# Kernel optimization log

Measured on AMD Instinct MI355X. Metric: run time of the kernel, lower is better.

## Reference

```python
import jax, jax.numpy as jnp
import numpy as np

DIM = 512; H = 8; DH = 64; M = 256; ITERS = 6; K = 33  # residual conv kernel


def _pinv(x, iters=ITERS):
    # Moore-Penrose iterative pseudo-inverse (lucidrains moore_penrose_iter_pinv)
    abs_x = jnp.abs(x)
    denom = abs_x.sum(-1).max() * abs_x.sum(-2).max()  # global max of col/row sums
    z = jnp.swapaxes(x, -1, -2) / denom
    I = jnp.eye(x.shape[-1], dtype=x.dtype)
    for _ in range(iters):
        xz = x @ z
        z = 0.25 * z @ (13. * I - xz @ (15. * I - xz @ (7. * I - xz)))
    return z


def setup_inputs() -> dict:
    key = jax.random.key(0)
    ks = jax.random.split(key, 5)
    b, n = 4, 4096
    inner = H * DH
    x = jax.random.normal(ks[0], (b, n, DIM), jnp.float32)
    ln_g = jnp.ones((DIM,), jnp.float32)
    ln_b = jnp.zeros((DIM,), jnp.float32)
    w_qkv = jax.random.normal(ks[1], (DIM, 3 * inner), jnp.float32) / np.sqrt(DIM).astype(np.float32)
    w_out = jax.random.normal(ks[2], (inner, DIM), jnp.float32) / np.sqrt(inner).astype(np.float32)
    b_out = jnp.zeros((DIM,), jnp.float32)
    res_w = jax.random.normal(ks[3], (H, K), jnp.float32) * 0.02  # depthwise conv weight per head
    return {"x": x, "ln_g": ln_g, "ln_b": ln_b, "w_qkv": w_qkv,
            "w_out": w_out, "b_out": b_out, "res_w": res_w}


def reference(x, ln_g, ln_b, w_qkv, w_out, b_out, res_w):
    b, n, d = x.shape
    # LayerNorm (eps=1e-5, biased variance, like torch)
    mu = x.mean(-1, keepdims=True)
    var = ((x - mu) ** 2).mean(-1, keepdims=True)
    xn = (x - mu) * jax.lax.rsqrt(var + 1e-5) * ln_g + ln_b
    # QKV projection, no bias
    qkv = xn @ w_qkv  # [b, n, 3*h*dh]
    q, k, v = jnp.split(qkv, 3, axis=-1)
    tohd = lambda t: t.reshape(b, n, H, DH).transpose(0, 2, 1, 3)  # b h n d
    q = tohd(q) * (DH ** -0.5)
    k = tohd(k)
    v = tohd(v)
    # landmarks: mean over consecutive blocks of l = n // M (n divisible by M here)
    l = n // M
    q_l = q.reshape(b, H, M, l, DH).mean(3)  # b h m d
    k_l = k.reshape(b, H, M, l, DH).mean(3)
    attn1 = jax.nn.softmax(jnp.einsum('bhid,bhjd->bhij', q, k_l), axis=-1)   # b h n m
    attn2 = jax.nn.softmax(jnp.einsum('bhid,bhjd->bhij', q_l, k_l), axis=-1)  # b h m m
    attn3 = jax.nn.softmax(jnp.einsum('bhid,bhjd->bhij', q_l, k), axis=-1)   # b h m n
    out = (attn1 @ _pinv(attn2)) @ (attn3 @ v)  # b h n dh
    # depthwise residual conv over sequence dim (Conv2d(heads, heads, (33,1), groups=heads))
    res = jax.lax.conv_general_dilated(
        v, res_w.reshape(H, 1, K, 1), (1, 1), ((K // 2, K // 2), (0, 0)),
        feature_group_count=H, dimension_numbers=('NCHW', 'OIHW', 'NCHW'))
    out = out + res
    # merge heads + output projection (dropout is identity at eval)
    out = out.transpose(0, 2, 1, 3).reshape(b, n, H * DH) @ w_out + b_out
    # TransLayer residual
    return x + out
```

## Files before the change

### kernel.cpp

```cpp
#include <hip/hip_runtime.h>
#include <hip/hip_bf16.h>

#define SEQ    4096
#define NBAT   4
#define NHEAD  8
#define NBH    32
#define DMODEL 512
#define DHEAD  64
#define NLM    256
#define NSP    4

typedef __attribute__((ext_vector_type(8))) short s8v;
typedef __attribute__((ext_vector_type(4))) float f4v;

__device__ __forceinline__ float b2f(unsigned short u){
  union { unsigned int i; float f; } v; v.i = ((unsigned int)u) << 16; return v.f;
}
__device__ __forceinline__ unsigned short f2b(float f){
  union { float f; unsigned int i; } v; v.f = f;
  unsigned int r = v.i + 0x7fffu + ((v.i >> 16) & 1u);
  return (unsigned short)(r >> 16);
}
__device__ __forceinline__ s8v ldg8(const unsigned short* p){
  return *reinterpret_cast<const s8v*>(p);
}
__device__ __forceinline__ f4v mfma16(s8v a, s8v b, f4v c){
  return __builtin_amdgcn_mfma_f32_16x16x32_bf16(a, b, c, 0, 0, 0);
}
__device__ __forceinline__ f4v zero4(){ f4v z; z[0]=0.f; z[1]=0.f; z[2]=0.f; z[3]=0.f; return z; }
__device__ __forceinline__ void gload16(const unsigned short* g, unsigned short* l){
  __builtin_amdgcn_global_load_lds((const __attribute__((address_space(1))) unsigned int*)g,
                                   (__attribute__((address_space(3))) unsigned int*)l, 16, 0, 0);
}

__global__ void k_prep(const float* __restrict__ wqkv, const float* __restrict__ wout,
                       unsigned short* __restrict__ wqkvT, unsigned short* __restrict__ woutT,
                       unsigned int* __restrict__ denomU){
  int t = blockIdx.x*256 + threadIdx.x;
  if (t == 0) denomU[0] = 0u;
  if (t < 786432){ int kk = t/1536, n = t%1536; wqkvT[(size_t)n*512 + kk] = f2b(wqkv[t]); }
  else { int t2 = t - 786432; if (t2 < 262144){ int kk = t2/512, n = t2%512; woutT[(size_t)n*512 + kk] = f2b(wout[t2]); } }
}

__global__ __launch_bounds__(256) void k_ln(const float* __restrict__ x, const float* __restrict__ g,
                                            const float* __restrict__ be, unsigned short* __restrict__ xn){
  int row = blockIdx.x*4 + (threadIdx.x>>6);
  int l = threadIdx.x & 63;
  const float* xr = x + (size_t)row*DMODEL;
  float4 a = *(const float4*)(xr + l*4);
  float4 b = *(const float4*)(xr + 256 + l*4);
  float s = a.x+a.y+a.z+a.w + b.x+b.y+b.z+b.w;
  float q = a.x*a.x+a.y*a.y+a.z*a.z+a.w*a.w + b.x*b.x+b.y*b.y+b.z*b.z+b.w*b.w;
  #pragma unroll
  for (int m=1;m<64;m<<=1){ s += __shfl_xor(s,m); q += __shfl_xor(q,m); }
  float mean = s*(1.f/DMODEL);
  float rstd = rsqrtf(q*(1.f/DMODEL) - mean*mean + 1e-5f);
  int c0 = l*4, c1 = 256 + l*4;
  float av[4] = {a.x,a.y,a.z,a.w}, bv[4] = {b.x,b.y,b.z,b.w};
  ushort4 u0, u1;
  unsigned short* p0 = (unsigned short*)&u0; unsigned short* p1 = (unsigned short*)&u1;
  #pragma unroll
  for (int e=0;e<4;++e){
    p0[e] = f2b((av[e]-mean)*rstd*g[c0+e] + be[c0+e]);
    p1[e] = f2b((bv[e]-mean)*rstd*g[c1+e] + be[c1+e]);
  }
  *(ushort4*)(xn + (size_t)row*DMODEL + c0) = u0;
  *(ushort4*)(xn + (size_t)row*DMODEL + c1) = u1;
}

__device__ __forceinline__ void gemm512v2(const unsigned short* __restrict__ A, const unsigned short* __restrict__ B,
                                          int m0, int n0, int t, unsigned short* lA, unsigned short* lB,
                                          f4v acc[4][4]){
  int w = t>>6, l = t&63;
  int wm = (w&1)*64, wn = (w>>1)*64;
  int g = l>>4, qi = l&15;
  int rs = (w<<4) + (l>>2);
  int s0 = l&3;
  int c0 = ((s0 ^ ((rs>>1)&3)) << 3);
  int r1 = rs + 64;
  int c1 = ((s0 ^ ((r1>>1)&3)) << 3);
  const unsigned short* gA0 = A + (size_t)(m0+rs)*DMODEL + c0;
  const unsigned short* gA1 = A + (size_t)(m0+r1)*DMODEL + c1;
  const unsigned short* gB0 = B + (size_t)(n0+rs)*DMODEL + c0;
  const unsigned short* gB1 = B + (size_t)(n0+r1)*DMODEL + c1;
  unsigned short* dA0 = lA + (w<<9);
  unsigned short* dA1 = lA + 2048 + (w<<9);
  unsigned short* dB0 = lB + (w<<9);
  unsigned short* dB1 = lB + 2048 + (w<<9);
  int aofs[4], bofs[4];
  #pragma unroll
  for (int i=0;i<4;++i){
    int ra = wm + i*16 + qi;
    aofs[i] = ra*32 + ((g ^ ((ra>>1)&3))<<3);
    int rb = wn + i*16 + qi;
    bofs[i] = rb*32 + ((g ^ ((rb>>1)&3))<<3);
  }
  for (int ks=0; ks<16; ++ks){
    gload16(gA0, dA0); gload16(gA1, dA1);
    gload16(gB0, dB0); gload16(gB1, dB1);
    gA0 += 32; gA1 += 32; gB0 += 32; gB1 += 32;
    __syncthreads();
    s8v af[4], bf[4];
    #pragma unroll
    for (int i=0;i<4;++i) af[i] = *(s8v*)&lA[aofs[i]];
    #pragma unroll
    for (int j=0;j<4;++j) bf[j] = *(s8v*)&lB[bofs[j]];
    #pragma unroll
    for (int i=0;i<4;++i)
      #pragma unroll
      for (int j=0;j<4;++j) acc[i][j] = mfma16(af[i], bf[j], acc[i][j]);
    __syncthreads();
  }
}

__global__ __launch_bounds__(256) void k_gqkv(const unsigned short* __restrict__ xn, const unsigned short* __restrict__ wT,
                                              unsigned short* __restrict__ q, unsigned short* __restrict__ k,
                                              unsigned short* __restrict__ v, unsigned short* __restrict__ vT){
  __shared__ __align__(16) unsigned short lA[4096], lB[4096];
  int b0 = blockIdx.x;
  int bid = (b0 & 7) * 192 + (b0 >> 3);
  int mblk = bid/12, nblk = bid%12;
  int m0 = mblk*128, n0 = nblk*128;
  int t = threadIdx.x;
  f4v acc[4][4];
  #pragma unroll
  for (int i=0;i<4;++i)
    #pragma unroll
    for (int j=0;j<4;++j) acc[i][j] = zero4();
  gemm512v2(xn, wT, m0, n0, t, lA, lB, acc);
  int w = t>>6, l = t&63; int wm = (w&1)*64, wn = (w>>1)*64;
  int part = nblk >> 2;
  int coff = (nblk & 3) * 128;
  unsigned short* dst = (part==0) ? q : (part==1) ? k : v;
  float scale = (part==0) ? 0.125f : 1.f;
  #pragma unroll
  for (int i=0;i<4;++i)
  #pragma unroll
  for (int j=0;j<4;++j){
    int colg = coff + wn + j*16 + (l&15);
    int h = colg>>6, c = colg&63;
    #pragma unroll
    for (int r=0;r<4;++r){
      int rowg = m0 + wm + i*16 + ((l>>4)<<2) + r;
      int b = rowg>>12, n = rowg&4095;
      unsigned short val = f2b(acc[i][j][r]*scale);
      dst[ (((size_t)(b*NHEAD + h))*SEQ + n)*DHEAD + c ] = val;
      if (part == 2)
        vT[ (((size_t)(b*NHEAD + h))*DHEAD + c)*SEQ + n ] = val;
    }
  }
}

__global__ __launch_bounds__(256) void k_gout(const unsigned short* __restrict__ ao, const unsigned short* __restrict__ wT,
                                              const float* __restrict__ x, const float* __restrict__ bo,
                                              float* __restrict__ out){
  __shared__ __align__(16) unsigned short lA[4096], lB[4096];
  int b0 = blockIdx.x;
  int bid = (b0 & 7) * 64 + (b0 >> 3);
  int mblk = bid>>2, nblk = bid&3;
  int m0 = mblk*128, n0 = nblk*128;
  int t = threadIdx.x;
  f4v acc[4][4];
  #pragma unroll
  for (int i=0;i<4;++i)
    #pragma unroll
    for (int j=0;j<4;++j) acc[i][j] = zero4();
  gemm512v2(ao, wT, m0, n0, t, lA, lB, acc);
  int w = t>>6, l = t&63; int wm = (w&1)*64, wn = (w>>1)*64;
  #pragma unroll
  for (int i=0;i<4;++i)
  #pragma unroll
  for (int j=0;j<4;++j){
    int colg = n0 + wn + j*16 + (l&15);
    #pragma unroll
    for (int r=0;r<4;++r){
      int rowg = m0 + wm + i*16 + ((l>>4)<<2) + r;
      size_t ad = (size_t)rowg*DMODEL + colg;
      out[ad] = acc[i][j][r] + x[ad] + bo[colg];
    }
  }
}

__global__ void k_lmk(const unsigned short* __restrict__ q, const unsigned short* __restrict__ k,
                      unsigned short* __restrict__ ql, unsigned short* __restrict__ kl){
  int tg = blockIdx.x*256 + threadIdx.x;
  int c4 = (tg&15)*4, m = (tg>>4)&255, bh = tg>>12;
  const unsigned short* qb = q + ((size_t)bh*SEQ + m*16)*DHEAD + c4;
  const unsigned short* kb = k + ((size_t)bh*SEQ + m*16)*DHEAD + c4;
  float s0=0.f,s1=0.f,s2=0.f,s3=0.f, t0=0.f,t1=0.f,t2=0.f,t3=0.f;
  #pragma unroll
  for (int j=0;j<16;++j){
    ushort4 uq = *(const ushort4*)(qb + (size_t)j*DHEAD);
    ushort4 uk = *(const ushort4*)(kb + (size_t)j*DHEAD);
    s0+=b2f(uq.x); s1+=b2f(uq.y); s2+=b2f(uq.z); s3+=b2f(uq.w);
    t0+=b2f(uk.x); t1+=b2f(uk.y); t2+=b2f(uk.z); t3+=b2f(uk.w);
  }
  ushort4 oq, ok;
  oq.x=f2b(s0*(1.f/16.f)); oq.y=f2b(s1*(1.f/16.f)); oq.z=f2b(s2*(1.f/16.f)); oq.w=f2b(s3*(1.f/16.f));
  ok.x=f2b(t0*(1.f/16.f)); ok.y=f2b(t1*(1.f/16.f)); ok.z=f2b(t2*(1.f/16.f)); ok.w=f2b(t3*(1.f/16.f));
  *(ushort4*)(ql + ((size_t)bh*NLM + m)*DHEAD + c4) = oq;
  *(ushort4*)(kl + ((size_t)bh*NLM + m)*DHEAD + c4) = ok;
}

__global__ __launch_bounds__(512) void k_attn2(const unsigned short* __restrict__ ql, const unsigned short* __restrict__ kl,
                                               unsigned short* __restrict__ a2, unsigned short* __restrict__ a2t,
                                               unsigned int* __restrict__ denomU){
  __shared__ float cs[256];
  int bh = blockIdx.x; int t = threadIdx.x; int w = t>>6, l = t&63;
  const unsigned short* Q = ql + (size_t)bh*NLM*DHEAD;
  const unsigned short* K = kl + (size_t)bh*NLM*DHEAD;
  f4v acc[2][16];
  #pragma unroll
  for (int i=0;i<2;++i)
    #pragma unroll
    for (int j=0;j<16;++j) acc[i][j] = zero4();
  int m0 = w*32;
  #pragma unroll
  for (int ks=0; ks<2; ++ks){
    int kk = ks*32 + ((l>>4)<<3);
    s8v af0 = ldg8(&Q[(size_t)(m0 + (l&15))*DHEAD + kk]);
    s8v af1 = ldg8(&Q[(size_t)(m0 + 16 + (l&15))*DHEAD + kk]);
    #pragma unroll
    for (int j=0;j<16;++j){
      s8v bf = ldg8(&K[(size_t)(j*16 + (l&15))*DHEAD + kk]);
      acc[0][j] = mfma16(af0, bf, acc[0][j]);
      acc[1][j] = mfma16(af1, bf, acc[1][j]);
    }
  }
  #pragma unroll
  for (int i=0;i<2;++i)
  #pragma unroll
  for (int r=0;r<4;++r){
    float mx = -1e30f;
    #pragma unroll
    for (int j=0;j<16;++j) mx = fmaxf(mx, acc[i][j][r]);
    #pragma unroll
    for (int mm=1;mm<16;mm<<=1) mx = fmaxf(mx, __shfl_xor(mx,mm));
    float sm = 0.f;
    #pragma unroll
    for (int j=0;j<16;++j){ float p = __expf(acc[i][j][r]-mx); acc[i][j][r]=p; sm += p; }
    #pragma unroll
    for (int mm=1;mm<16;mm<<=1) sm += __shfl_xor(sm,mm);
    float inv = 1.f/sm;
    #pragma unroll
    for (int j=0;j<16;++j) acc[i][j][r] *= inv;
  }
  for (int e=t; e<256; e+=512) cs[e] = 0.f;
  __syncthreads();
  size_t b0 = (size_t)bh*NLM*NLM;
  #pragma unroll
  for (int i=0;i<2;++i)
  #pragma unroll
  for (int j=0;j<16;++j){
    int col = j*16 + (l&15);
    int rowb = m0 + i*16 + ((l>>4)<<2);
    float csp = 0.f;
    #pragma unroll
    for (int r=0;r<4;++r){
      float p = acc[i][j][r];
      unsigned short pb = f2b(p);
      a2 [b0 + (size_t)(rowb+r)*NLM + col] = pb;
      a2t[b0 + (size_t)col*NLM + rowb + r] = pb;
      csp += p;
    }
    csp += __shfl_xor(csp, 16); csp += __shfl_xor(csp, 32);
    if ((l>>4) == 0) atomicAdd(&cs[col], csp);
  }
  __syncthreads();
  if (t < 256) atomicMax(denomU, __float_as_uint(cs[t]));
}

__global__ __launch_bounds__(256) void k_a3w2p(const unsigned short* __restrict__ ql, const unsigned short* __restrict__ kb,
                                               const unsigned short* __restrict__ vT,
                                               float* __restrict__ po, float* __restrict__ pm, float* __restrict__ pd){
  __shared__ __align__(16) unsigned short Ks[256*64];
  __shared__ __align__(16) unsigned short Vs[64*256];
  int bid = blockIdx.x;
  int ksp = bid & 3;
  int qp  = (bid >> 2) & 3;
  int bh  = bid >> 4;
  int t = threadIdx.x, w = t>>6, l = t&63;
  int q0 = qp*64 + w*16;
  int g = l>>4, qi = l&15;
  const unsigned short* Q = ql + ((size_t)bh*NLM + q0)*DHEAD;
  const unsigned short* K = kb + (size_t)bh*SEQ*DHEAD;
  const unsigned short* V = vT + (size_t)bh*DHEAD*SEQ;
  s8v bq0 = ldg8(&Q[(size_t)qi*DHEAD + g*8]);
  s8v bq1 = ldg8(&Q[(size_t)qi*DHEAD + 32 + g*8]);
  float m_run = -1e30f, den = 0.f;
  f4v oacc[4];
  #pragma unroll
  for (int j=0;j<4;++j) oacc[j] = zero4();
  int sl0 = ((g&1)*2)*16 + qi;
  int jsel = g>>1;
  for (int kc = ksp*4; kc < ksp*4+4; ++kc){
    const unsigned short* Kc = K + (size_t)kc*256*DHEAD;
    #pragma unroll
    for (int it2=0; it2<8; ++it2){
      int cid = it2*256 + t;
      int row = cid>>3, cl = cid&7;
      gload16(&Kc[(size_t)(row<<6) + ((cl^(row&7))<<3)], Ks + it2*2048 + w*512);
      int row2 = cid>>5, cl2 = cid&31;
      gload16(&V[(size_t)row2*SEQ + kc*256 + ((cl2^(row2&7))<<3)], Vs + it2*2048 + 16384 - 16384 + w*512 + 0);
    }
    __syncthreads();
    f4v acc[16];
    #pragma unroll
    for (int j=0;j<16;++j) acc[j] = zero4();
    #pragma unroll
    for (int ks=0;ks<2;++ks){
      s8v bq = (ks==0) ? bq0 : bq1;
      #pragma unroll
      for (int j=0;j<16;++j){
        int r = j*16+qi;
        s8v ak = *(s8v*)&Ks[(size_t)(r<<6) + (((ks*4+g) ^ (qi&7))<<3)];
        acc[j] = mfma16(ak, bq, acc[j]);
      }
    }
    float cm = -1e30f;
    #pragma unroll
    for (int j=0;j<16;++j)
      cm = fmaxf(cm, fmaxf(fmaxf(acc[j][0],acc[j][1]), fmaxf(acc[j][2],acc[j][3])));
    cm = fmaxf(cm, __shfl_xor(cm,16));
    cm = fmaxf(cm, __shfl_xor(cm,32));
    float nm = fmaxf(m_run, cm);
    float f = __expf(m_run - nm);
    m_run = nm;
    float ls = 0.f;
    unsigned int pku[32];
    #pragma unroll
    for (int j=0;j<16;++j){
      float p0 = __expf(acc[j][0]-nm), p1 = __expf(acc[j][1]-nm);
      float p2 = __expf(acc[j][2]-nm), p3 = __expf(acc[j][3]-nm);
      ls += (p0+p1)+(p2+p3);
      pku[2*j+0] = (unsigned int)f2b(p0) | ((unsigned int)f2b(p1)<<16);
      pku[2*j+1] = (unsigned int)f2b(p2) | ((unsigned int)f2b(p3)<<16);
    }
    den = den*f + ls;
    float fr0 = __shfl(f, g*4+0, 64), fr1 = __shfl(f, g*4+1, 64);
    float fr2 = __shfl(f, g*4+2, 64), fr3 = __shfl(f, g*4+3, 64);
    #pragma unroll
    for (int j=0;j<4;++j){
      oacc[j][0]*=fr0; oacc[j][1]*=fr1; oacc[j][2]*=fr2; oacc[j][3]*=fr3;
    }
    #pragma unroll
    for (int ks=0;ks<8;++ks){
      unsigned int w0a = (unsigned int)__shfl((int)pku[4*ks+0], sl0, 64);
      unsigned int w1a = (unsigned int)__shfl((int)pku[4*ks+1], sl0, 64);
      unsigned int w0b = (unsigned int)__shfl((int)pku[4*ks+2], sl0, 64);
      unsigned int w1b = (unsigned int)__shfl((int)pku[4*ks+3], sl0, 64);
      unsigned int w2a = (unsigned int)__shfl((int)pku[4*ks+0], sl0+16, 64);
      unsigned int w3a = (unsigned int)__shfl((int)pku[4*ks+1], sl0+16, 64);
      unsigned int w2b = (unsigned int)__shfl((int)pku[4*ks+2], sl0+16, 64);
      unsigned int w3b = (unsigned int)__shfl((int)pku[4*ks+3], sl0+16, 64);
      unsigned int wv0 = jsel ? w0b : w0a;
      unsigned int wv1 = jsel ? w1b : w1a;
      unsigned int wv2 = jsel ? w2b : w2a;
      unsigned int wv3 = jsel ? w3b : w3a;
      s8v af;
      af[0] = (short)(wv0&0xffff); af[1] = (short)(wv0>>16);
      af[2] = (short)(wv1&0xffff); af[3] = (short)(wv1>>16);
      af[4] = (short)(wv2&0xffff); af[5] = (short)(wv2>>16);
      af[6] = (short)(wv3&0xffff); af[7] = (short)(wv3>>16);
      int ch = ks*4 + g;
      #pragma unroll
      for (int j=0;j<4;++j){
        int r = j*16+qi;
        s8v bu = *(s8v*)&Vs[(size_t)(r<<8) + ((ch ^ (qi&7))<<3)];
        oacc[j] = mfma16(af, bu, oacc[j]);
      }
    }
    __syncthreads();
  }
  den += __shfl_xor(den,16); den += __shfl_xor(den,32);
  #pragma unroll
  for (int j=0;j<4;++j)
    #pragma unroll
    for (int r=0;r<4;++r)
      po[(((size_t)(ksp*NBH + bh))*NLM + q0 + g*4 + r)*DHEAD + j*16 + qi] = oacc[j][r];
  if (g == 0){
    pm[(size_t)(ksp*NBH + bh)*NLM + q0 + qi] = m_run;
    pd[(size_t)(ksp*NBH + bh)*NLM + q0 + qi] = den;
  }
}

__global__ __launch_bounds__(256) void k_a3c(const float* __restrict__ po, const float* __restrict__ pm,
                                             const float* __restrict__ pd, unsigned short* __restrict__ w2t){
  int tg = blockIdx.x*256 + threadIdx.x;
  int bh = tg >> 12; int c = (tg >> 6) & 63; int r4 = (tg & 63) << 2;
  ushort4 ov;
  unsigned short* op = (unsigned short*)&ov;
  #pragma unroll
  for (int rr=0; rr<4; ++rr){
    int row = r4 + rr;
    float m[NSP];
    float gm = -1e30f;
    #pragma unroll
    for (int s=0;s<NSP;++s){ m[s] = pm[(size_t)(s*NBH+bh)*NLM + row]; gm = fmaxf(gm, m[s]); }
    float den = 0.f, o = 0.f;
    #pragma unroll
    for (int s=0;s<NSP;++s){
      float wsc = __expf(m[s]-gm);
      den += pd[(size_t)(s*NBH+bh)*NLM + row]*wsc;
      o   += po[(((size_t)(s*NBH+bh))*NLM + row)*DHEAD + c]*wsc;
    }
    op[rr] = f2b(o/den);
  }
  *(ushort4*)&w2t[(size_t)bh*DHEAD*NLM + (size_t)c*NLM + r4] = ov;
}

__global__ __launch_bounds__(256) void k_conv(const unsigned short* __restrict__ v, const float* __restrict__ rw,
                                              unsigned short* __restrict__ cf){
  int bh = blockIdx.x >> 6;
  int n0 = (blockIdx.x & 63) * 64;
  int h = bh & 7, b = bh >> 3;
  int t = threadIdx.x;
  int tx = t & 15, ty = t >> 4;
  int c4 = tx * 4;
  int nb = n0 + ty * 4;
  const unsigned short* vb = v + ((size_t)bh * SEQ) * DHEAD + c4;
  ushort4 val[36];
  #pragma unroll
  for (int i = 0; i < 36; ++i){
    int nn = nb - 16 + i;
    if (nn >= 0 && nn < SEQ) val[i] = *(const ushort4*)(vb + (size_t)nn * DHEAD);
    else { val[i].x = 0; val[i].y = 0; val[i].z = 0; val[i].w = 0; }
  }
  float wgt[33];
  #pragma unroll
  for (int o = 0; o < 33; ++o) wgt[o] = rw[h*33 + o];
  #pragma unroll
  for (int i = 0; i < 4; ++i){
    float s0 = 0.f, s1 = 0.f, s2 = 0.f, s3 = 0.f;
    #pragma unroll
    for (int o = 0; o < 33; ++o){
      ushort4 u = val[i + o];
      float w0 = wgt[o];
      s0 += w0 * b2f(u.x); s1 += w0 * b2f(u.y);
      s2 += w0 * b2f(u.z); s3 += w0 * b2f(u.w);
    }
    ushort4 ov;
    ov.x = f2b(s0); ov.y = f2b(s1); ov.z = f2b(s2); ov.w = f2b(s3);
    size_t ad = ((size_t)b * SEQ + (nb + i)) * DMODEL + h * DHEAD + c4;
    *(ushort4*)(cf + ad) = ov;
  }
}

__device__ __forceinline__ void pcore(const unsigned short* __restrict__ Ab, const unsigned short* __restrict__ Bb,
                                      int m0, int n0, int l, f4v acc[4][4]){
  for (int ks=0; ks<8; ++ks){
    int kk = ks*32 + ((l>>4)<<3);
    s8v af[4], bf[4];
    #pragma unroll
    for (int i=0;i<4;++i) af[i] = ldg8(&Ab[(size_t)(m0 + i*16 + (l&15))*256 + kk]);
    #pragma unroll
    for (int j=0;j<4;++j) bf[j] = ldg8(&Bb[(size_t)(n0 + j*16 + (l&15))*256 + kk]);
    #pragma unroll
    for (int i=0;i<4;++i)
      #pragma unroll
      for (int j=0;j<4;++j) acc[i][j] = mfma16(af[i], bf[j], acc[i][j]);
  }
}

__global__ __launch_bounds__(64) void k_pg1(const unsigned short* __restrict__ A, const unsigned short* __restrict__ BT,
                                            unsigned short* __restrict__ oN, unsigned short* __restrict__ oT,
                                            int sdiv, const unsigned int* __restrict__ denomU){
  int bid = blockIdx.x;
  int bh = bid>>4, tt = bid&15;
  int m0 = (tt>>2)*64, n0 = (tt&3)*64;
  int l = threadIdx.x;
  const unsigned short* Ab = A + (size_t)bh*65536;
  const unsigned short* Bb = BT + (size_t)bh*65536;
  f4v acc[4][4];
  #pragma unroll
  for (int i=0;i<4;++i)
    #pragma unroll
    for (int j=0;j<4;++j) acc[i][j] = zero4();
  pcore(Ab, Bb, m0, n0, l, acc);
  float s = sdiv ? 1.f/__uint_as_float(denomU[0]) : 1.f;
  #pragma unroll
  for (int i=0;i<4;++i)
  #pragma unroll
  for (int j=0;j<4;++j){
    int col = n0 + j*16 + (l&15);
    #pragma unroll
    for (int r=0;r<4;++r){
      int row = m0 + i*16 + ((l>>4)<<2) + r;
      unsigned short ob = f2b(acc[i][j][r]*s);
      oN[(size_t)bh*65536 + (size_t)row*256 + col] = ob;
      oT[(size_t)bh*65536 + (size_t)col*256 + row] = ob;
    }
  }
}

__global__ __launch_bounds__(64) void k_pg2(const unsigned short* __restrict__ xzN, const unsigned short* __restrict__ xzT,
                                            const unsigned short* __restrict__ zsrc,
                                            unsigned short* __restrict__ CT, unsigned short* __restrict__ PN,
                                            int sdiv, const unsigned int* __restrict__ denomU){
  int bid = blockIdx.x;
  int part = bid>>9; bid &= 511;
  int bh = bid>>4, tt = bid&15;
  int m0 = (tt>>2)*64, n0 = (tt&3)*64;
  int l = threadIdx.x;
  const unsigned short* Ab = (part==0 ? xzN : zsrc) + (size_t)bh*65536;
  const unsigned short* Bb = xzT + (size_t)bh*65536;
  f4v acc[4][4];
  #pragma unroll
  for (int i=0;i<4;++i)
    #pragma unroll
    for (int j=0;j<4;++j) acc[i][j] = zero4();
  pcore(Ab, Bb, m0, n0, l, acc);
  if (part == 0){
    #pragma unroll
    for (int i=0;i<4;++i)
    #pragma unroll
    for (int j=0;j<4;++j){
      int col = n0 + j*16 + (l&15);
      #pragma unroll
      for (int r=0;r<4;++r){
        int row = m0 + i*16 + ((l>>4)<<2) + r;
        float xv = b2f(xzN[(size_t)bh*65536 + (size_t)row*256 + col]);
        CT[(size_t)bh*65536 + (size_t)col*256 + row] = f2b(7.f*xv - acc[i][j][r]);
      }
    }
  } else {
    float s = sdiv ? 1.f/__uint_as_float(denomU[0]) : 1.f;
    #pragma unroll
    for (int i=0;i<4;++i)
    #pragma unroll
    for (int j=0;j<4;++j){
      int col = n0 + j*16 + (l&15);
      #pragma unroll
      for (int r=0;r<4;++r){
        int row = m0 + i*16 + ((l>>4)<<2) + r;
        PN[(size_t)bh*65536 + (size_t)row*256 + col] = f2b(acc[i][j][r]*s);
      }
    }
  }
}

__global__ __launch_bounds__(64) void k_pg3(const unsigned short* __restrict__ PN, const unsigned short* __restrict__ CT,
                                            const unsigned short* __restrict__ zsrc,
                                            unsigned short* __restrict__ zN, unsigned short* __restrict__ zT,
                                            int sdiv, const unsigned int* __restrict__ denomU){
  int bid = blockIdx.x;
  int bh = bid>>4, tt = bid&15;
  int m0 = (tt>>2)*64, n0 = (tt&3)*64;
  int l = threadIdx.x;
  const unsigned short* Ab = PN + (size_t)bh*65536;
  const unsigned short* Bb = CT + (size_t)bh*65536;
  f4v acc[4][4];
  #pragma unroll
  for (int i=0;i<4;++i)
    #pragma unroll
    for (int j=0;j<4;++j) acc[i][j] = zero4();
  pcore(Ab, Bb, m0, n0, l, acc);
  float zs = sdiv ? 1.f/__uint_as_float(denomU[0]) : 1.f;
  #pragma unroll
  for (int i=0;i<4;++i)
  #pragma unroll
  for (int j=0;j<4;++j){
    int col = n0 + j*16 + (l&15);
    #pragma unroll
    for (int r=0;r<4;++r){
      int row = m0 + i*16 + ((l>>4)<<2) + r;
      float zv = b2f(zsrc[(size_t)bh*65536 + (size_t)row*256 + col])*zs;
      float pv = b2f(PN  [(size_t)bh*65536 + (size_t)row*256 + col]);
      float res = 0.25f*(13.f*zv - 15.f*pv + acc[i][j][r]);
      unsigned short ob = f2b(res);
      zN[(size_t)bh*65536 + (size_t)row*256 + col] = ob;
      zT[(size_t)bh*65536 + (size_t)col*256 + row] = ob;
    }
  }
}

template<bool WN, bool WT>
__global__ __launch_bounds__(64) void k_pgemm(
    const unsigned short* __restrict__ A, const unsigned short* __restrict__ BT,
    unsigned short* __restrict__ oN, unsigned short* __restrict__ oT,
    int mt, int nt, long strA, long strBT, long strON, long strOT)
{
  int bid = blockIdx.x;
  int nper = mt*nt;
  int bh = bid/nper, tt = bid%nper;
  int m0 = (tt/nt)*64, n0 = (tt%nt)*64;
  const unsigned short* Ab = A + (size_t)bh*strA;
  const unsigned short* Bb = BT + (size_t)bh*strBT;
  int l = threadIdx.x;
  f4v acc[4][4];
  #pragma unroll
  for (int i=0;i<4;++i)
    #pragma unroll
    for (int j=0;j<4;++j) acc[i][j] = zero4();
  pcore(Ab, Bb, m0, n0, l, acc);
  #pragma unroll
  for (int i=0;i<4;++i)
  #pragma unroll
  for (int j=0;j<4;++j){
    int col = n0 + j*16 + (l&15);
    #pragma unroll
    for (int r=0;r<4;++r){
      int row = m0 + i*16 + ((l>>4)<<2) + r;
      unsigned short ob = f2b(acc[i][j][r]);
      if constexpr (WN) oN[(size_t)bh*strON + (size_t)row*256 + col] = ob;
      if constexpr (WT) oT[(size_t)bh*strOT + (size_t)col*256 + row] = ob;
    }
  }
}

__global__ __launch_bounds__(256) void k_attn1(const unsigned short* __restrict__ qb, const unsigned short* __restrict__ kl,
                                               const unsigned short* __restrict__ ut, const unsigned short* __restrict__ cf,
                                               unsigned short* __restrict__ ao){
  int bh = blockIdx.x>>6;
  int t = threadIdx.x, w = t>>6, l = t&63;
  int q0 = ((blockIdx.x&63)<<6) + (w<<4);
  int g = l>>4, qi = l&15;
  const unsigned short* Q = qb + (size_t)bh*SEQ*DHEAD;
  const unsigned short* K = kl + (size_t)bh*NLM*DHEAD;
  f4v acc[16];
  #pragma unroll
  for (int j=0;j<16;++j) acc[j] = zero4();
  #pragma unroll
  for (int ks=0;ks<2;++ks){
    int kk = ks*32 + g*8;
    s8v bq = ldg8(&Q[(size_t)(q0+qi)*DHEAD + kk]);
    #pragma unroll
    for (int j=0;j<16;++j){
      s8v ak = ldg8(&K[(size_t)(j*16+qi)*DHEAD + kk]);
      acc[j] = mfma16(ak, bq, acc[j]);
    }
  }
  float mx = -1e30f;
  #pragma unroll
  for (int j=0;j<16;++j)
    mx = fmaxf(mx, fmaxf(fmaxf(acc[j][0],acc[j][1]), fmaxf(acc[j][2],acc[j][3])));
  mx = fmaxf(mx, __shfl_xor(mx,16));
  mx = fmaxf(mx, __shfl_xor(mx,32));
  float sm = 0.f;
  #pragma unroll
  for (int j=0;j<16;++j)
    #pragma unroll
    for (int r=0;r<4;++r){ float p = __expf(acc[j][r]-mx); acc[j][r]=p; sm += p; }
  sm += __shfl_xor(sm,16); sm += __shfl_xor(sm,32);
  float inv = 1.f/sm;
  unsigned int pku[32];
  #pragma unroll
  for (int j=0;j<16;++j){
    pku[2*j+0] = (unsigned int)f2b(acc[j][0]*inv) | ((unsigned int)f2b(acc[j][1]*inv)<<16);
    pku[2*j+1] = (unsigned int)f2b(acc[j][2]*inv) | ((unsigned int)f2b(acc[j][3]*inv)<<16);
  }
  const unsigned short* U = ut + (size_t)bh*DHEAD*NLM;
  f4v oacc[4];
  #pragma unroll
  for (int j=0;j<4;++j) oacc[j] = zero4();
  int sl0 = ((g&1)*2)*16 + qi;
  int jsel = g>>1;
  #pragma unroll
  for (int ks=0;ks<8;++ks){
    unsigned int w0a = (unsigned int)__shfl((int)pku[4*ks+0], sl0, 64);
    unsigned int w1a = (unsigned int)__shfl((int)pku[4*ks+1], sl0, 64);
    unsigned int w0b = (unsigned int)__shfl((int)pku[4*ks+2], sl0, 64);
    unsigned int w1b = (unsigned int)__shfl((int)pku[4*ks+3], sl0, 64);
    unsigned int w2a = (unsigned int)__shfl((int)pku[4*ks+0], sl0+16, 64);
    unsigned int w3a = (unsigned int)__shfl((int)pku[4*ks+1], sl0+16, 64);
    unsigned int w2b = (unsigned int)__shfl((int)pku[4*ks+2], sl0+16, 64);
    unsigned int w3b = (unsigned int)__shfl((int)pku[4*ks+3], sl0+16, 64);
    unsigned int wv0 = jsel ? w0b : w0a;
    unsigned int wv1 = jsel ? w1b : w1a;
    unsigned int wv2 = jsel ? w2b : w2a;
    unsigned int wv3 = jsel ? w3b : w3a;
    s8v af;
    af[0] = (short)(wv0&0xffff); af[1] = (short)(wv0>>16);
    af[2] = (short)(wv1&0xffff); af[3] = (short)(wv1>>16);
    af[4] = (short)(wv2&0xffff); af[5] = (short)(wv2>>16);
    af[6] = (short)(wv3&0xffff); af[7] = (short)(wv3>>16);
    int mk = ks*32 + g*8;
    #pragma unroll
    for (int j=0;j<4;++j){
      s8v bu = ldg8(&U[(size_t)(j*16+qi)*NLM + mk]);
      oacc[j] = mfma16(af, bu, oacc[j]);
    }
  }
  int b = bh>>3, h = bh&7;
  #pragma unroll
  for (int j=0;j<4;++j){
    int c = j*16 + qi;
    #pragma unroll
    for (int r=0;r<4;++r){
      int n = q0 + g*4 + r;
      size_t ad = ((size_t)(b*SEQ + n))*DMODEL + h*DHEAD + c;
      ao[ad] = f2b(oacc[j][r] + b2f(cf[ad]));
    }
  }
}

extern "C" void kernel_launch(void* const* d_in, const int* in_sizes, int n_in,
                              void* d_out, int out_size, void* d_ws, size_t ws_size,
                              hipStream_t stream){
  const float* x    = (const float*)d_in[0];
  const float* lng  = (const float*)d_in[1];
  const float* lnb  = (const float*)d_in[2];
  const float* wqkv = (const float*)d_in[3];
  const float* wout = (const float*)d_in[4];
  const float* bout = (const float*)d_in[5];
  const float* resw = (const float*)d_in[6];
  float* out = (float*)d_out;

  char* ws = (char*)d_ws;
  size_t off = 0;
  auto alloc = [&](size_t bytes)->char*{ char* p = ws + off; off += (bytes + 255) & ~(size_t)255; return p; };

  unsigned short* wqkvT = (unsigned short*)alloc((size_t)1536*512*2);
  unsigned short* woutT = (unsigned short*)alloc((size_t)512*512*2);
  unsigned int*   denomU= (unsigned int*)  alloc(256);
  unsigned short* xn    = (unsigned short*)alloc((size_t)16384*512*2);
  unsigned short* zA  = xn;
  unsigned short* zAT = xn + (size_t)1*NBH*NLM*NLM;
  unsigned short* zB  = xn + (size_t)2*NBH*NLM*NLM;
  unsigned short* zBT = xn + (size_t)3*NBH*NLM*NLM;
  unsigned short* q   = (unsigned short*)alloc((size_t)NBH*SEQ*DHEAD*2);
  unsigned short* kb  = (unsigned short*)alloc((size_t)NBH*SEQ*DHEAD*2);
  unsigned short* ao  = kb;
  unsigned short* v   = (unsigned short*)alloc((size_t)NBH*SEQ*DHEAD*2);
  unsigned short* vT  = (unsigned short*)alloc((size_t)NBH*DHEAD*SEQ*2);
  unsigned short* ql  = (unsigned short*)alloc((size_t)NBH*NLM*DHEAD*2);
  unsigned short* kl  = (unsigned short*)alloc((size_t)NBH*NLM*DHEAD*2);
  unsigned short* a2  = (unsigned short*)alloc((size_t)NBH*NLM*NLM*2);
  unsigned short* a2t = (unsigned short*)alloc((size_t)NBH*NLM*NLM*2);
  unsigned short* convf = (unsigned short*)alloc((size_t)NBAT*SEQ*DMODEL*2);
  unsigned short* xzN = (unsigned short*)alloc((size_t)NBH*NLM*NLM*2);
  unsigned short* xzT = (unsigned short*)alloc((size_t)NBH*NLM*NLM*2);
  unsigned short* pn  = (unsigned short*)alloc((size_t)NBH*NLM*NLM*2);
  unsigned short* ctb = (unsigned short*)alloc((size_t)NBH*NLM*NLM*2);
  float* po = (float*)alloc((size_t)NSP*NBH*NLM*DHEAD*4);
  float* pm = (float*)alloc((size_t)NSP*NBH*NLM*4);
  float* pd = (float*)alloc((size_t)NSP*NBH*NLM*4);
  unsigned short* w2t = (unsigned short*)alloc((size_t)NBH*DHEAD*NLM*2);
  unsigned short* ut  = (unsigned short*)alloc((size_t)NBH*DHEAD*NLM*2);
  (void)ws_size; (void)in_sizes; (void)n_in; (void)out_size;

  k_prep<<<4096,256,0,stream>>>(wqkv, wout, wqkvT, woutT, denomU);
  k_ln  <<<4096,256,0,stream>>>(x, lng, lnb, xn);
  k_gqkv<<<1536,256,0,stream>>>(xn, wqkvT, q, kb, v, vT);
  k_lmk <<<512,256,0,stream>>>(q, kb, ql, kl);
  k_attn2<<<32,512,0,stream>>>(ql, kl, a2, a2t, denomU);
  k_a3w2p<<<512,256,0,stream>>>(ql, kb, vT, po, pm, pd);
  k_a3c <<<512,256,0,stream>>>(po, pm, pd, w2t);
  k_conv<<<2048,256,0,stream>>>(v, resw, convf);

  unsigned short* zN_[2] = {zA, zB};
  unsigned short* zT_[2] = {zAT, zBT};
  for (int it = 0; it < 6; ++it){
    const unsigned short* BT   = (it==0) ? a2  : zT_[(it-1)&1];
    const unsigned short* zsrc = (it==0) ? a2t : zN_[(it-1)&1];
    int sdiv = (it==0) ? 1 : 0;
    k_pg1<<<512 ,64,0,stream>>>(a2, BT, xzN, xzT, sdiv, denomU);
    k_pg2<<<1024,64,0,stream>>>(xzN, xzT, zsrc, ctb, pn, sdiv, denomU);
    k_pg3<<<512 ,64,0,stream>>>(pn, ctb, zsrc, zN_[it&1], zT_[it&1], sdiv, denomU);
  }
  k_pgemm<false,true><<<128,64,0,stream>>>(zN_[1], w2t, (unsigned short*)nullptr, ut, 4,1, 65536L,16384L,0L,16384L);

  k_attn1<<<2048,256,0,stream>>>(q, kl, ut, convf, ao);
  k_gout <<<512,256,0,stream>>>(ao, woutT, x, bout, out);
}
```

Measured before the change: 459.0 us.

## Restructure pinv iteration to track X=A·Z recurrence with two-kernel steps

Reformulates the Newton-Schulz pseudo-inverse so each iteration updates both the product X=A·Z (scaled) and Z in two fused launches instead of three. The dependent GEMM chain per iteration becomes shorter, and the denominator scale is folded into the initial X and the final U=Z·W2 kernel. It costs extra intermediate buffers and more GEMMs per launch. Keeping A·Z as its own recurrence in bf16 may also shift rounding behaviour.

```diff
diff --git a/kernel.cpp b/kernel.cpp
--- a/kernel.cpp
+++ b/kernel.cpp
@@ -462,22 +462,22 @@
   }
 }
 
-__global__ __launch_bounds__(64) void k_pg1(const unsigned short* __restrict__ A, const unsigned short* __restrict__ BT,
-                                            unsigned short* __restrict__ oN, unsigned short* __restrict__ oT,
-                                            int sdiv, const unsigned int* __restrict__ denomU){
+
+__global__ __launch_bounds__(64) void k_x0(const unsigned short* __restrict__ a2,
+                                           unsigned short* __restrict__ XN, unsigned short* __restrict__ XT,
+                                           const unsigned int* __restrict__ denomU){
   int bid = blockIdx.x;
   int bh = bid>>4, tt = bid&15;
   int m0 = (tt>>2)*64, n0 = (tt&3)*64;
   int l = threadIdx.x;
-  const unsigned short* Ab = A + (size_t)bh*65536;
-  const unsigned short* Bb = BT + (size_t)bh*65536;
+  size_t bb = (size_t)bh*65536;
   f4v acc[4][4];
   #pragma unroll
   for (int i=0;i<4;++i)
     #pragma unroll
     for (int j=0;j<4;++j) acc[i][j] = zero4();
-  pcore(Ab, Bb, m0, n0, l, acc);
-  float s = sdiv ? 1.f/__uint_as_float(denomU[0]) : 1.f;
+  pcore(a2+bb, a2+bb, m0, n0, l, acc);
+  float s = 1.f/__uint_as_float(denomU[0]);
   #pragma unroll
   for (int i=0;i<4;++i)
   #pragma unroll
@@ -487,30 +487,30 @@
     for (int r=0;r<4;++r){
       int row = m0 + i*16 + ((l>>4)<<2) + r;
       unsigned short ob = f2b(acc[i][j][r]*s);
-      oN[(size_t)bh*65536 + (size_t)row*256 + col] = ob;
-      oT[(size_t)bh*65536 + (size_t)col*256 + row] = ob;
-    }
-  }
-}
-
-__global__ __launch_bounds__(64) void k_pg2(const unsigned short* __restrict__ xzN, const unsigned short* __restrict__ xzT,
-                                            const unsigned short* __restrict__ zsrc,
-                                            unsigned short* __restrict__ CT, unsigned short* __restrict__ PN,
-                                            int sdiv, const unsigned int* __restrict__ denomU){
+      XN[bb + (size_t)row*256 + col] = ob;
+      XT[bb + (size_t)col*256 + row] = ob;
+    }
+  }
+}
+
+__global__ __launch_bounds__(64) void k_l1(const unsigned short* __restrict__ XN, const unsigned short* __restrict__ XT,
+                                           const unsigned short* __restrict__ zsrc,
+                                           unsigned short* __restrict__ YN, unsigned short* __restrict__ YT,
+                                           unsigned short* __restrict__ CT,
+                                           unsigned short* __restrict__ WN, unsigned short* __restrict__ EN){
   int bid = blockIdx.x;
   int part = bid>>9; bid &= 511;
   int bh = bid>>4, tt = bid&15;
   int m0 = (tt>>2)*64, n0 = (tt&3)*64;
   int l = threadIdx.x;
-  const unsigned short* Ab = (part==0 ? xzN : zsrc) + (size_t)bh*65536;
-  const unsigned short* Bb = xzT + (size_t)bh*65536;
+  size_t bb = (size_t)bh*65536;
   f4v acc[4][4];
   #pragma unroll
   for (int i=0;i<4;++i)
     #pragma unroll
     for (int j=0;j<4;++j) acc[i][j] = zero4();
-  pcore(Ab, Bb, m0, n0, l, acc);
   if (part == 0){
+    pcore(XN+bb, XT+bb, m0, n0, l, acc);
     #pragma unroll
     for (int i=0;i<4;++i)
     #pragma unroll
@@ -519,12 +519,16 @@
       #pragma unroll
       for (int r=0;r<4;++r){
         int row = m0 + i*16 + ((l>>4)<<2) + r;
-        float xv = b2f(xzN[(size_t)bh*65536 + (size_t)row*256 + col]);
-        CT[(size_t)bh*65536 + (size_t)col*256 + row] = f2b(7.f*xv - acc[i][j][r]);
+        float y = acc[i][j][r];
+        float xv = b2f(XN[bb + (size_t)row*256 + col]);
+        unsigned short yb = f2b(y);
+        YN[bb + (size_t)row*256 + col] = yb;
+        YT[bb + (size_t)col*256 + row] = yb;
+        CT[bb + (size_t)col*256 + row] = f2b(7.f*xv - y);
       }
     }
   } else {
-    float s = sdiv ? 1.f/__uint_as_float(denomU[0]) : 1.f;
+    pcore(zsrc+bb, XT+bb, m0, n0, l, acc);
     #pragma unroll
     for (int i=0;i<4;++i)
     #pragma unroll
@@ -533,77 +537,93 @@
       #pragma unroll
       for (int r=0;r<4;++r){
         int row = m0 + i*16 + ((l>>4)<<2) + r;
-        PN[(size_t)bh*65536 + (size_t)row*256 + col] = f2b(acc[i][j][r]*s);
+        size_t idx = bb + (size_t)row*256 + col;
+        float wv = acc[i][j][r];
+        float zv = b2f(zsrc[idx]);
+        WN[idx] = f2b(wv);
+        EN[idx] = f2b(7.f*zv - wv);
       }
     }
   }
 }
 
-__global__ __launch_bounds__(64) void k_pg3(const unsigned short* __restrict__ PN, const unsigned short* __restrict__ CT,
-                                            const unsigned short* __restrict__ zsrc,
-                                            unsigned short* __restrict__ zN, unsigned short* __restrict__ zT,
-                                            int sdiv, const unsigned int* __restrict__ denomU){
+__global__ __launch_bounds__(64) void k_l2(unsigned short* __restrict__ XN, unsigned short* __restrict__ XT,
+                                           const unsigned short* __restrict__ zsrc, unsigned short* __restrict__ zdst,
+                                           const unsigned short* __restrict__ YN, const unsigned short* __restrict__ YT,
+                                           const unsigned short* __restrict__ CT,
+                                           const unsigned short* __restrict__ WN, const unsigned short* __restrict__ EN,
+                                           int zonly){
   int bid = blockIdx.x;
+  int part;
+  if (zonly){ part = 1; } else { part = bid>>9; bid &= 511; }
   int bh = bid>>4, tt = bid&15;
   int m0 = (tt>>2)*64, n0 = (tt&3)*64;
   int l = threadIdx.x;
-  const unsigned short* Ab = PN + (size_t)bh*65536;
-  const unsigned short* Bb = CT + (size_t)bh*65536;
+  size_t bb = (size_t)bh*65536;
   f4v acc[4][4];
   #pragma unroll
   for (int i=0;i<4;++i)
     #pragma unroll
     for (int j=0;j<4;++j) acc[i][j] = zero4();
-  pcore(Ab, Bb, m0, n0, l, acc);
-  float zs = sdiv ? 1.f/__uint_as_float(denomU[0]) : 1.f;
+  if (part == 0){
+    pcore(YN+bb, CT+bb, m0, n0, l, acc);
+    #pragma unroll
+    for (int i=0;i<4;++i)
+    #pragma unroll
+    for (int j=0;j<4;++j){
+      int col = n0 + j*16 + (l&15);
+      #pragma unroll
+      for (int r=0;r<4;++r){
+        int row = m0 + i*16 + ((l>>4)<<2) + r;
+        size_t idx = bb + (size_t)row*256 + col;
+        float xv = b2f(XN[idx]);
+        float yv = b2f(YN[idx]);
+        unsigned short ob = f2b(0.25f*(13.f*xv - 15.f*yv + acc[i][j][r]));
+        XN[idx] = ob;
+        XT[bb + (size_t)col*256 + row] = ob;
+      }
+    }
+  } else {
+    pcore(EN+bb, YT+bb, m0, n0, l, acc);
+    #pragma unroll
+    for (int i=0;i<4;++i)
+    #pragma unroll
+    for (int j=0;j<4;++j){
+      int col = n0 + j*16 + (l&15);
+      #pragma unroll
+      for (int r=0;r<4;++r){
+        int row = m0 + i*16 + ((l>>4)<<2) + r;
+        size_t idx = bb + (size_t)row*256 + col;
+        float zv = b2f(zsrc[idx]);
+        float wv = b2f(WN[idx]);
+        zdst[idx] = f2b(0.25f*(13.f*zv - 15.f*wv + acc[i][j][r]));
+      }
+    }
+  }
+}
+
+__global__ __launch_bounds__(64) void k_ue(const unsigned short* __restrict__ z6, const unsigned short* __restrict__ w2t,
+                                           unsigned short* __restrict__ ut, const unsigned int* __restrict__ denomU){
+  int bid = blockIdx.x;
+  int bh = bid>>2, tt = bid&3;
+  int m0 = tt*64;
+  int l = threadIdx.x;
+  float dinv = 1.f/__uint_as_float(denomU[0]);
+  f4v acc[4][4];
+  #pragma unroll
+  for (int i=0;i<4;++i)
+    #pragma unroll
+    for (int j=0;j<4;++j) acc[i][j] = zero4();
+  pcore(z6 + (size_t)bh*65536, w2t + (size_t)bh*16384, m0, 0, l, acc);
   #pragma unroll
   for (int i=0;i<4;++i)
   #pragma unroll
   for (int j=0;j<4;++j){
-    int col = n0 + j*16 + (l&15);
+    int col = j*16 + (l&15);
     #pragma unroll
     for (int r=0;r<4;++r){
       int row = m0 + i*16 + ((l>>4)<<2) + r;
-      float zv = b2f(zsrc[(size_t)bh*65536 + (size_t)row*256 + col])*zs;
-      float pv = b2f(PN  [(size_t)bh*65536 + (size_t)row*256 + col]);
-      float res = 0.25f*(13.f*zv - 15.f*pv + acc[i][j][r]);
-      unsigned short ob = f2b(res);
-      zN[(size_t)bh*65536 + (size_t)row*256 + col] = ob;
-      zT[(size_t)bh*65536 + (size_t)col*256 + row] = ob;
-    }
-  }
-}
-
-template<bool WN, bool WT>
-__global__ __launch_bounds__(64) void k_pgemm(
-    const unsigned short* __restrict__ A, const unsigned short* __restrict__ BT,
-    unsigned short* __restrict__ oN, unsigned short* __restrict__ oT,
-    int mt, int nt, long strA, long strBT, long strON, long strOT)
-{
-  int bid = blockIdx.x;
-  int nper = mt*nt;
-  int bh = bid/nper, tt = bid%nper;
-  int m0 = (tt/nt)*64, n0 = (tt%nt)*64;
-  const unsigned short* Ab = A + (size_t)bh*strA;
-  const unsigned short* Bb = BT + (size_t)bh*strBT;
-  int l = threadIdx.x;
-  f4v acc[4][4];
-  #pragma unroll
-  for (int i=0;i<4;++i)
-    #pragma unroll
-    for (int j=0;j<4;++j) acc[i][j] = zero4();
-  pcore(Ab, Bb, m0, n0, l, acc);
-  #pragma unroll
-  for (int i=0;i<4;++i)
-  #pragma unroll
-  for (int j=0;j<4;++j){
-    int col = n0 + j*16 + (l&15);
-    #pragma unroll
-    for (int r=0;r<4;++r){
-      int row = m0 + i*16 + ((l>>4)<<2) + r;
-      unsigned short ob = f2b(acc[i][j][r]);
-      if constexpr (WN) oN[(size_t)bh*strON + (size_t)row*256 + col] = ob;
-      if constexpr (WT) oT[(size_t)bh*strOT + (size_t)col*256 + row] = ob;
+      ut[(size_t)bh*16384 + (size_t)col*256 + row] = f2b(acc[i][j][r]*dinv);
     }
   }
 }
@@ -714,10 +734,10 @@
   unsigned short* woutT = (unsigned short*)alloc((size_t)512*512*2);
   unsigned int*   denomU= (unsigned int*)  alloc(256);
   unsigned short* xn    = (unsigned short*)alloc((size_t)16384*512*2);
-  unsigned short* zA  = xn;
-  unsigned short* zAT = xn + (size_t)1*NBH*NLM*NLM;
-  unsigned short* zB  = xn + (size_t)2*NBH*NLM*NLM;
-  unsigned short* zBT = xn + (size_t)3*NBH*NLM*NLM;
+  unsigned short* XN = xn;
+  unsigned short* XT = xn + (size_t)1*NBH*NLM*NLM;
+  unsigned short* YN = xn + (size_t)2*NBH*NLM*NLM;
+  unsigned short* YT = xn + (size_t)3*NBH*NLM*NLM;
   unsigned short* q   = (unsigned short*)alloc((size_t)NBH*SEQ*DHEAD*2);
   unsigned short* kb  = (unsigned short*)alloc((size_t)NBH*SEQ*DHEAD*2);
   unsigned short* ao  = kb;
@@ -728,10 +748,11 @@
   unsigned short* a2  = (unsigned short*)alloc((size_t)NBH*NLM*NLM*2);
   unsigned short* a2t = (unsigned short*)alloc((size_t)NBH*NLM*NLM*2);
   unsigned short* convf = (unsigned short*)alloc((size_t)NBAT*SEQ*DMODEL*2);
-  unsigned short* xzN = (unsigned short*)alloc((size_t)NBH*NLM*NLM*2);
-  unsigned short* xzT = (unsigned short*)alloc((size_t)NBH*NLM*NLM*2);
-  unsigned short* pn  = (unsigned short*)alloc((size_t)NBH*NLM*NLM*2);
-  unsigned short* ctb = (unsigned short*)alloc((size_t)NBH*NLM*NLM*2);
+  unsigned short* CTb = (unsigned short*)alloc((size_t)NBH*NLM*NLM*2);
+  unsigned short* WN  = (unsigned short*)alloc((size_t)NBH*NLM*NLM*2);
+  unsigned short* EN  = (unsigned short*)alloc((size_t)NBH*NLM*NLM*2);
+  unsigned short* zP  = (unsigned short*)alloc((size_t)NBH*NLM*NLM*2);
+  unsigned short* zQ  = (unsigned short*)alloc((size_t)NBH*NLM*NLM*2);
   float* po = (float*)alloc((size_t)NSP*NBH*NLM*DHEAD*4);
   float* pm = (float*)alloc((size_t)NSP*NBH*NLM*4);
   float* pd = (float*)alloc((size_t)NSP*NBH*NLM*4);
@@ -748,17 +769,16 @@
   k_a3c <<<512,256,0,stream>>>(po, pm, pd, w2t);
   k_conv<<<2048,256,0,stream>>>(v, resw, convf);
 
-  unsigned short* zN_[2] = {zA, zB};
-  unsigned short* zT_[2] = {zAT, zBT};
+  k_x0<<<512,64,0,stream>>>(a2, XN, XT, denomU);
+  unsigned short* zbuf[2] = {zP, zQ};
+  const unsigned short* zs = a2t;
   for (int it = 0; it < 6; ++it){
-    const unsigned short* BT   = (it==0) ? a2  : zT_[(it-1)&1];
-    const unsigned short* zsrc = (it==0) ? a2t : zN_[(it-1)&1];
-    int sdiv = (it==0) ? 1 : 0;
-    k_pg1<<<512 ,64,0,stream>>>(a2, BT, xzN, xzT, sdiv, denomU);
-    k_pg2<<<1024,64,0,stream>>>(xzN, xzT, zsrc, ctb, pn, sdiv, denomU);
-    k_pg3<<<512 ,64,0,stream>>>(pn, ctb, zsrc, zN_[it&1], zT_[it&1], sdiv, denomU);
-  }
-  k_pgemm<false,true><<<128,64,0,stream>>>(zN_[1], w2t, (unsigned short*)nullptr, ut, 4,1, 65536L,16384L,0L,16384L);
+    int zonly = (it==5) ? 1 : 0;
+    k_l1<<<1024,64,0,stream>>>(XN, XT, zs, YN, YT, CTb, WN, EN);
+    k_l2<<<zonly?512:1024,64,0,stream>>>(XN, XT, zs, zbuf[it&1], YN, YT, CTb, WN, EN, zonly);
+    zs = zbuf[it&1];
+  }
+  k_ue<<<128,64,0,stream>>>(zs, w2t, ut, denomU);
 
   k_attn1<<<2048,256,0,stream>>>(q, kl, ut, convf, ao);
   k_gout <<<512,256,0,stream>>>(ao, woutT, x, bout, out);
```

Measured after the change: 566.5 us. 1.23x slower.
